# Kernel optimization log

Hardware: AMD Instinct MI355X
Metric: run time of the kernel (lower is better)

Reference implementation:

```python
import jax, jax.numpy as jnp
import numpy as np

# ---- static config (from init_kwargs) ----
B_, L_, DM = 4, 2048, 1024
EXPAND, HEADDIM, DSTATE, DCONV = 2, 64, 64, 7
DIN = EXPAND * DM            # 2048
NH = DIN // HEADDIM          # 32
CONV_DIM = DIN + 2 * DSTATE  # 2176 (x, B, C go through the depthwise conv)
DPROJ = 2 * DIN + 2 * DSTATE + 2 * NH  # 4288 (z, xBC, dt_fwd, dt_bwd)
EPS = 1e-5


def setup_inputs() -> dict:
    key = jax.random.key(0)
    ks = jax.random.split(key, 8)
    s = lambda d: 1.0 / np.sqrt(d)
    # dt_bias = inv_softplus(dt) with dt ~ logUniform(1e-3, 0.1)  (Mamba2/Hydra init)
    dt = jnp.exp(jax.random.uniform(ks[3], (NH,)) * (np.log(0.1) - np.log(0.001)) + np.log(0.001))
    return {
        "x": jax.random.normal(ks[0], (B_, L_, DM), jnp.float32),
        "ln_gamma": jnp.ones((DM,), jnp.float32),
        "ln_beta": jnp.zeros((DM,), jnp.float32),
        "W_in": jax.random.normal(ks[1], (DPROJ, DM), jnp.float32) * s(DM),
        "conv_w": jax.random.normal(ks[2], (CONV_DIM, DCONV), jnp.float32) * s(DCONV),
        "conv_b": jnp.zeros((CONV_DIM,), jnp.float32),
        "dt_bias": jnp.log(jnp.expm1(dt)),
        "A_log": jnp.log(jax.random.uniform(ks[4], (NH,), minval=1.0, maxval=16.0)),
        "fc_D_w": jax.random.normal(ks[5], (NH, DIN), jnp.float32) * s(DIN),
        "D": jnp.ones((NH,), jnp.float32),
        "norm_w": jnp.ones((DIN,), jnp.float32),
        "W_out": jax.random.normal(ks[6], (DM, DIN), jnp.float32) * s(DIN),
    }


def _hydra_layer(x, ln_gamma, ln_beta, W_in, conv_w, conv_b, dt_bias, A_log,
                 fc_D_w, D, norm_w, W_out):
    res = x
    # LayerNorm
    mu = jnp.mean(x, -1, keepdims=True)
    var = jnp.mean((x - mu) ** 2, -1, keepdims=True)
    u = (x - mu) * jax.lax.rsqrt(var + EPS) * ln_gamma + ln_beta

    # input projection -> z (gate), xBC (conv stream), dt (fwd+bwd)
    zxbcdt = jnp.einsum('bld,pd->blp', u, W_in)
    z = zxbcdt[..., :DIN]
    xBC = zxbcdt[..., DIN:DIN + CONV_DIM]
    dt = zxbcdt[..., DIN + CONV_DIM:]               # (B,L,2*NH)

    # depthwise 'same' conv along L + SiLU (bidirectional model -> symmetric pad)
    xBC_c = jax.lax.conv_general_dilated(
        xBC.transpose(0, 2, 1), conv_w[:, None, :], (1,),
        [(DCONV // 2, DCONV // 2)], feature_group_count=CONV_DIM)
    xBC = jax.nn.silu((xBC_c + conv_b[None, :, None]).transpose(0, 2, 1))

    xs = xBC[..., :DIN]                             # (B,L,DIN)
    Bm = xBC[..., DIN:DIN + DSTATE]                 # (B,L,N)
    Cm = xBC[..., DIN + DSTATE:]                    # (B,L,N)

    flip = lambda a: a[:, ::-1]
    # stack forward and (flipped) backward direction along batch
    dt2 = jax.nn.softplus(jnp.concatenate([dt[..., :NH], flip(dt[..., NH:])], 0) + dt_bias)  # (2B,L,NH)
    x2 = jnp.concatenate([xs, flip(xs)], 0).reshape(2 * B_, L_, NH, HEADDIM)
    B2 = jnp.concatenate([Bm, flip(Bm)], 0)
    C2 = jnp.concatenate([Cm, flip(Cm)], 0)

    A = -jnp.exp(A_log)                             # (NH,)
    dA = jnp.exp(dt2 * A)                           # (2B,L,NH)

    # selective SSM recurrence: h_t = dA_t * h_{t-1} + dt_t * x_t B_t^T ; y_t = h_t C_t
    def step(h, inp):
        dA_t, dt_t, B_t, C_t, x_t = inp
        dBx = (dt_t[:, :, None, None] * x_t[..., None]) * B_t[:, None, None, :]
        h = dA_t[:, :, None, None] * h + dBx        # (2B,NH,P,N)
        y = jnp.einsum('bhpn,bn->bhp', h, C_t)
        return h, y

    h0 = jnp.zeros((2 * B_, NH, HEADDIM, DSTATE), x.dtype)
    tr = lambda a: jnp.moveaxis(a, 1, 0)
    _, ys = jax.lax.scan(step, h0, (tr(dA), tr(dt2), tr(B2), tr(C2), tr(x2)))
    y = jnp.moveaxis(ys, 0, 1)                      # (2B,L,NH,P)

    # shift by one: strictly off-diagonal part of the quasiseparable mixing matrix
    y = jnp.concatenate([jnp.zeros_like(y[:, :1]), y[:, :-1]], axis=1)
    y = y[:B_] + flip(y[B_:])                       # (B,L,NH,P)

    # data-dependent diagonal: D(x) = fc_D(x) + D, applied per head
    Ddata = jnp.einsum('bld,hd->blh', xs, fc_D_w) + D
    y = y + xs.reshape(B_, L_, NH, HEADDIM) * Ddata[..., None]
    y = y.reshape(B_, L_, DIN)

    # gated RMSNorm (norm after gate)
    y = y * jax.nn.silu(z)
    y = y * jax.lax.rsqrt(jnp.mean(y * y, -1, keepdims=True) + EPS) * norm_w

    # out proj + residual (dropout is identity in eval)
    return res + jnp.einsum('bli,di->bld', y, W_out)


def reference(x, ln_gamma, ln_beta, W_in, conv_w, conv_b, dt_bias, A_log,
              fc_D_w, D, norm_w, W_out):
    return _hydra_layer(x, ln_gamma, ln_beta, W_in, conv_w, conv_b, dt_bias,
                        A_log, fc_D_w, D, norm_w, W_out)
```

## Files before the change

kernel.cpp:

```cpp
#include <hip/hip_runtime.h>
#include <stdint.h>

#define B_   4
#define L_   2048
#define DM   1024
#define DIN  2048
#define NH   32
#define HD   64
#define DSTATE 64
#define DCONV  7
#define CONV_DIM 2176
#define DPROJ 4288
#define NPAD 4352
#define BL   8192
#define EPS  1e-5f
#define QC   128
#define NCH  16

typedef unsigned short u16;
typedef unsigned int   u32;
typedef __bf16 bf16x8 __attribute__((ext_vector_type(8)));
typedef float  f32x4  __attribute__((ext_vector_type(4)));

__device__ __forceinline__ float b2f(u32 b) { return __uint_as_float(b << 16); }
__device__ __forceinline__ u16 f2b(float f) {
    u32 u = __float_as_uint(f);
    u32 r = (u + 0x7fffu + ((u >> 16) & 1u)) >> 16;
    return (u16)r;
}
__device__ __forceinline__ void unpack8(uint4 v, float* f) {
    f[0] = b2f(v.x & 0xffffu); f[1] = b2f(v.x >> 16);
    f[2] = b2f(v.y & 0xffffu); f[3] = b2f(v.y >> 16);
    f[4] = b2f(v.z & 0xffffu); f[5] = b2f(v.z >> 16);
    f[6] = b2f(v.w & 0xffffu); f[7] = b2f(v.w >> 16);
}
__device__ __forceinline__ uint4 pack8(const float* f) {
    uint4 v;
    v.x = (u32)f2b(f[0]) | ((u32)f2b(f[1]) << 16);
    v.y = (u32)f2b(f[2]) | ((u32)f2b(f[3]) << 16);
    v.z = (u32)f2b(f[4]) | ((u32)f2b(f[5]) << 16);
    v.w = (u32)f2b(f[6]) | ((u32)f2b(f[7]) << 16);
    return v;
}
__device__ __forceinline__ int xts(int p, int s) { return p * 136 + ((p >> 3) << 3) + s; }
__device__ __forceinline__ void gload_lds16(const u16* g, u16* l) {
    __builtin_amdgcn_global_load_lds((const __attribute__((address_space(1))) void*)g,
                                     (__attribute__((address_space(3))) void*)l, 16, 0, 0);
}

__global__ __launch_bounds__(256) void k_cvt_win(const float* __restrict__ W, u16* __restrict__ Wb) {
    int idx = blockIdx.x * 256 + threadIdx.x;
    int n = idx >> 10;
    float v = (n < DPROJ) ? W[(size_t)n * DM + (idx & 1023)] : 0.f;
    Wb[idx] = f2b(v);
}
__global__ __launch_bounds__(256) void k_cvt_wout(const float* __restrict__ W, u16* __restrict__ Wb) {
    int idx = blockIdx.x * 256 + threadIdx.x;
    Wb[idx] = f2b(W[idx]);
}
__global__ __launch_bounds__(256) void k_cvt_fcd(const float* __restrict__ W, u16* __restrict__ Wb) {
    int idx = blockIdx.x * 256 + threadIdx.x;
    Wb[idx] = f2b(W[idx]);
}

__global__ __launch_bounds__(256) void k_ln(const float* __restrict__ x, const float* __restrict__ g,
                                            const float* __restrict__ be, u16* __restrict__ u) {
    int row = blockIdx.x, tid = threadIdx.x;
    const float4* xr = (const float4*)(x + (size_t)row * DM);
    float4 v = xr[tid];
    float s1 = v.x + v.y + v.z + v.w;
    float s2 = v.x * v.x + v.y * v.y + v.z * v.z + v.w * v.w;
    for (int o = 32; o; o >>= 1) { s1 += __shfl_down(s1, o); s2 += __shfl_down(s2, o); }
    __shared__ float ls1[4], ls2[4];
    int w = tid >> 6;
    if ((tid & 63) == 0) { ls1[w] = s1; ls2[w] = s2; }
    __syncthreads();
    float t1 = ls1[0] + ls1[1] + ls1[2] + ls1[3];
    float t2 = ls2[0] + ls2[1] + ls2[2] + ls2[3];
    float mu = t1 * (1.f / DM);
    float var = t2 * (1.f / DM) - mu * mu;
    float rs = rsqrtf(var + EPS);
    float4 gv = ((const float4*)g)[tid];
    float4 bv = ((const float4*)be)[tid];
    float o0 = (v.x - mu) * rs * gv.x + bv.x;
    float o1 = (v.y - mu) * rs * gv.y + bv.y;
    float o2 = (v.z - mu) * rs * gv.z + bv.z;
    float o3 = (v.w - mu) * rs * gv.w + bv.w;
    uint2 p;
    p.x = (u32)f2b(o0) | ((u32)f2b(o1) << 16);
    p.y = (u32)f2b(o2) | ((u32)f2b(o3) << 16);
    ((uint2*)(u + (size_t)row * DM))[tid] = p;
}

__global__ __launch_bounds__(256) void k_gemm_bt(const u16* __restrict__ A, const u16* __restrict__ Bw,
                                                 int M, int N, int K, int out_bf16,
                                                 u16* __restrict__ obf, int ldo,
                                                 float* __restrict__ ofp, const float* __restrict__ res) {
    __shared__ __align__(16) u16 As[128 * 64];
    __shared__ __align__(16) u16 Bs[128 * 64];
    int tid = threadIdx.x;
    int m0 = blockIdx.y * 128, n0 = blockIdx.x * 128;
    int w = tid >> 6, lane = tid & 63;
    int wm = (w >> 1) * 64, wn = (w & 1) * 64;
    int lr = lane & 15, lq = lane >> 4;

    f32x4 acc[4][4];
    #pragma unroll
    for (int i = 0; i < 4; i++)
        #pragma unroll
        for (int j = 0; j < 4; j++) acc[i][j] = (f32x4){0.f, 0.f, 0.f, 0.f};

    for (int kt = 0; kt < K; kt += 64) {
        #pragma unroll
        for (int it = 0; it < 4; it++) {
            int s_idx = it * 256 + tid;
            int row = s_idx >> 3;
            int kcg = (s_idx & 7) ^ (row & 7);
            u16* lbase_a = &As[(it * 256 + w * 64) * 8];
            u16* lbase_b = &Bs[(it * 256 + w * 64) * 8];
            gload_lds16(A + (size_t)(m0 + row) * K + kt + kcg * 8, lbase_a);
            gload_lds16(Bw + (size_t)(n0 + row) * K + kt + kcg * 8, lbase_b);
        }
        __syncthreads();
        #pragma unroll
        for (int kk = 0; kk < 2; kk++) {
            bf16x8 af[4], bfr[4];
            #pragma unroll
            for (int i = 0; i < 4; i++) {
                int row = wm + 16 * i + lr;
                af[i] = *(const bf16x8*)&As[row * 64 + (((kk * 4 + lq)) ^ (row & 7)) * 8];
            }
            #pragma unroll
            for (int j = 0; j < 4; j++) {
                int row = wn + 16 * j + lr;
                bfr[j] = *(const bf16x8*)&Bs[row * 64 + (((kk * 4 + lq)) ^ (row & 7)) * 8];
            }
            #pragma unroll
            for (int i = 0; i < 4; i++)
                #pragma unroll
                for (int j = 0; j < 4; j++)
                    acc[i][j] = __builtin_amdgcn_mfma_f32_16x16x32_bf16(af[i], bfr[j], acc[i][j], 0, 0, 0);
        }
        __syncthreads();
    }
    #pragma unroll
    for (int i = 0; i < 4; i++) {
        #pragma unroll
        for (int j = 0; j < 4; j++) {
            #pragma unroll
            for (int rr = 0; rr < 4; rr++) {
                int m = m0 + wm + 16 * i + lq * 4 + rr;
                int n = n0 + wn + 16 * j + lr;
                float v = acc[i][j][rr];
                if (out_bf16) obf[(size_t)m * ldo + n] = f2b(v);
                else          ofp[(size_t)m * ldo + n] = v + res[(size_t)m * ldo + n];
            }
        }
    }
}

__global__ __launch_bounds__(256) void k_dproj(const u16* __restrict__ xs, const u16* __restrict__ fcb,
                                               const float* __restrict__ Dv, float* __restrict__ Dd) {
    __shared__ __align__(16) u16 As[32 * 72];
    __shared__ __align__(16) u16 Bs[32 * 72];
    int tid = threadIdx.x;
    int m0 = blockIdx.x * 32;
    int w = tid >> 6, lane = tid & 63, lr = lane & 15, lq = lane >> 4;
    int mt = (w & 1) * 16, nt = (w >> 1) * 16;
    int r = tid >> 3, kc = tid & 7;
    f32x4 acc = (f32x4){0.f, 0.f, 0.f, 0.f};
    for (int kt = 0; kt < DIN; kt += 64) {
        *(uint4*)&As[r * 72 + kc * 8] = *(const uint4*)(xs + (size_t)(m0 + r) * DIN + kt + kc * 8);
        *(uint4*)&Bs[r * 72 + kc * 8] = *(const uint4*)(fcb + (size_t)r * DIN + kt + kc * 8);
        __syncthreads();
        #pragma unroll
        for (int ks = 0; ks < 2; ks++) {
            bf16x8 a = *(const bf16x8*)&As[(mt + lr) * 72 + ks * 32 + lq * 8];
            bf16x8 b = *(const bf16x8*)&Bs[(nt + lr) * 72 + ks * 32 + lq * 8];
            acc = __builtin_amdgcn_mfma_f32_16x16x32_bf16(a, b, acc, 0, 0, 0);
        }
        __syncthreads();
    }
    #pragma unroll
    for (int rr = 0; rr < 4; rr++) {
        int m = m0 + mt + lq * 4 + rr;
        int n = nt + lr;
        Dd[(size_t)m * 32 + n] = acc[rr] + Dv[n];
    }
}

__global__ __launch_bounds__(256) void k_conv(const u16* __restrict__ zx, const float* __restrict__ cw,
                                              const float* __restrict__ cb, u16* __restrict__ xs,
                                              u16* __restrict__ BCb) {
    __shared__ u16 sh[262 * 64];
    int c0 = blockIdx.x * 64, t0 = blockIdx.y * 256, b = blockIdx.z;
    int tid = threadIdx.x;
    int c = tid & 63, tg = tid >> 6;
    for (int it = 0; it < 66; it++) {
        int r = it * 4 + tg;
        if (r < 262) {
            int t = t0 + r - 3;
            u16 v = 0;
            if (t >= 0 && t < L_) v = zx[(size_t)(b * L_ + t) * NPAD + DIN + c0 + c];
            sh[r * 64 + c] = v;
        }
    }
    float wgt[7];
    #pragma unroll
    for (int k = 0; k < 7; k++) wgt[k] = cw[(c0 + c) * 7 + k];
    float bias = cb[c0 + c];
    __syncthreads();
    int cg = c0 + c;
    for (int tt = 0; tt < 64; tt++) {
        int tl = tt * 4 + tg;
        float a = bias;
        #pragma unroll
        for (int k = 0; k < 7; k++) a += b2f(sh[(tl + k) * 64 + c]) * wgt[k];
        float v = a / (1.f + __expf(-a));
        size_t row = (size_t)b * L_ + (t0 + tl);
        if (cg < DIN) xs[row * DIN + cg] = f2b(v);
        else          BCb[row * 128 + (cg - DIN)] = f2b(v);
    }
}

__global__ __launch_bounds__(256) void k_chunk(const u16* __restrict__ xs, const u16* __restrict__ BCb,
                                               const u16* __restrict__ zx, const float* __restrict__ dt_bias,
                                               const float* __restrict__ A_log, u16* __restrict__ y0,
                                               u16* __restrict__ y1, float* __restrict__ wout,
                                               float* __restrict__ decay, u16* __restrict__ scb) {
    __shared__ __align__(16) u16 ab[18432];
    __shared__ __align__(16) u16 XT[8768];
    __shared__ __align__(16) u16 BT[8768];
    __shared__ __align__(16) float dts_s[128];
    __shared__ __align__(16) float lda_s[128];
    __shared__ __align__(16) float wend[128];
    __shared__ __align__(16) double cumd[128];

    const int blk = blockIdx.x;
    const int c = blk & 15, dbh = blk >> 4;
    const int h = dbh & 31, b = (dbh >> 5) & 3, dir = dbh >> 7;
    const int tid = threadIdx.x, w = tid >> 6, lane = tid & 63, lr = lane & 15, lq = lane >> 4;
    const int s0 = c * QC;
    u16* yo = dir ? y1 : y0;

    if (tid < 128) {
        int s = s0 + tid;
        int t = dir ? (L_ - 1 - s) : s;
        float draw = b2f(zx[(size_t)(b * L_ + t) * NPAD + (DIN + CONV_DIM) + dir * 32 + h]);
        float xb = draw + dt_bias[h];
        float dt2 = (xb > 20.f) ? xb : log1pf(__expf(xb));
        dts_s[tid] = dt2;
        lda_s[tid] = -__expf(A_log[h]) * dt2;
    }
    {
        int sl0 = tid >> 3, ng = (tid & 7) * 8;
        #pragma unroll
        for (int it = 0; it < 4; it++) {
            int sl = sl0 + it * 32;
            int s = s0 + sl;
            int t = dir ? (L_ - 1 - s) : s;
            size_t row = (size_t)b * L_ + t;
            const u16* bcr = BCb + row * 128;
            uint4 cv = *(const uint4*)(bcr + 64 + ng);
            *(uint4*)&ab[sl * 72 + ng] = cv;
            uint4 pb = *(const uint4*)(bcr + ng);
            *(uint4*)&ab[9216 + sl * 72 + ng] = pb;
            u16 bh[8] = {(u16)(pb.x & 0xffffu), (u16)(pb.x >> 16), (u16)(pb.y & 0xffffu), (u16)(pb.y >> 16),
                         (u16)(pb.z & 0xffffu), (u16)(pb.z >> 16), (u16)(pb.w & 0xffffu), (u16)(pb.w >> 16)};
            #pragma unroll
            for (int i = 0; i < 8; i++) BT[(ng + i) * 136 + ng + sl] = bh[i];
            uint4 xv = *(const uint4*)(xs + row * DIN + h * 64 + ng);
            u16 xh[8] = {(u16)(xv.x & 0xffffu), (u16)(xv.x >> 16), (u16)(xv.y & 0xffffu), (u16)(xv.y >> 16),
                         (u16)(xv.z & 0xffffu), (u16)(xv.z >> 16), (u16)(xv.w & 0xffffu), (u16)(xv.w >> 16)};
            #pragma unroll
            for (int i = 0; i < 8; i++) XT[(ng + i) * 136 + ng + sl] = xh[i];
        }
    }
    __syncthreads();
    if (w == 0) {
        double v0 = (double)lda_s[lane];
        double v1 = (double)lda_s[64 + lane];
        #pragma unroll
        for (int o = 1; o < 64; o <<= 1) {
            double t0 = __shfl_up(v0, o);
            double t1 = __shfl_up(v1, o);
            if (lane >= o) { v0 += t0; v1 += t1; }
        }
        double tot0 = __shfl(v0, 63);
        cumd[lane] = v0;
        cumd[64 + lane] = tot0 + v1;
    }
    bf16x8 af[2][2];
    #pragma unroll
    for (int ti = 0; ti < 2; ti++)
        #pragma unroll
        for (int ks = 0; ks < 2; ks++)
            af[ti][ks] = *(const bf16x8*)&ab[(w * 32 + ti * 16 + lr) * 72 + ks * 32 + lq * 8];
    f32x4 accg[2][8];
    #pragma unroll
    for (int ti = 0; ti < 2; ti++)
        #pragma unroll
        for (int si = 0; si < 8; si++) accg[ti][si] = (f32x4){0.f, 0.f, 0.f, 0.f};
    #pragma unroll
    for (int si = 0; si < 8; si++)
        #pragma unroll
        for (int ks = 0; ks < 2; ks++) {
            bf16x8 bf = *(const bf16x8*)&ab[9216 + (si * 16 + lr) * 72 + ks * 32 + lq * 8];
            accg[0][si] = __builtin_amdgcn_mfma_f32_16x16x32_bf16(af[0][ks], bf, accg[0][si], 0, 0, 0);
            accg[1][si] = __builtin_amdgcn_mfma_f32_16x16x32_bf16(af[1][ks], bf, accg[1][si], 0, 0, 0);
        }
    __syncthreads();
    if (tid < 128) wend[tid] = __expf((float)(cumd[127] - cumd[tid])) * dts_s[tid];
    {
        double cumt_d[8];
        #pragma unroll
        for (int ti = 0; ti < 2; ti++)
            #pragma unroll
            for (int r = 0; r < 4; r++) cumt_d[ti * 4 + r] = cumd[w * 32 + ti * 16 + lq * 4 + r];
        double cums_d[8]; float dts_l[8];
        #pragma unroll
        for (int si = 0; si < 8; si++) { cums_d[si] = cumd[si * 16 + lr]; dts_l[si] = dts_s[si * 16 + lr]; }
        #pragma unroll
        for (int ti = 0; ti < 2; ti++)
            #pragma unroll
            for (int si = 0; si < 8; si++)
                #pragma unroll
                for (int r = 0; r < 4; r++) {
                    int t_l = w * 32 + ti * 16 + lq * 4 + r;
                    int s_l = si * 16 + lr;
                    float v = 0.f;
                    if (s_l <= t_l)
                        v = __expf((float)(cumt_d[ti * 4 + r] - cums_d[si])) * dts_l[si] * accg[ti][si][r];
                    ab[xts(t_l, s_l)] = f2b(v);
                }
    }
    __syncthreads();
    f32x4 acc[2][4];
    #pragma unroll
    for (int ti = 0; ti < 2; ti++)
        #pragma unroll
        for (int pj = 0; pj < 4; pj++) acc[ti][pj] = (f32x4){0.f, 0.f, 0.f, 0.f};
    #pragma unroll
    for (int ks = 0; ks < 4; ks++) {
        bf16x8 a0 = *(const bf16x8*)&ab[xts(w * 32 + lr, ks * 32 + lq * 8)];
        bf16x8 a1 = *(const bf16x8*)&ab[xts(w * 32 + 16 + lr, ks * 32 + lq * 8)];
        #pragma unroll
        for (int pj = 0; pj < 4; pj++) {
            bf16x8 bf = *(const bf16x8*)&XT[xts(pj * 16 + lr, ks * 32 + lq * 8)];
            acc[0][pj] = __builtin_amdgcn_mfma_f32_16x16x32_bf16(a0, bf, acc[0][pj], 0, 0, 0);
            acc[1][pj] = __builtin_amdgcn_mfma_f32_16x16x32_bf16(a1, bf, acc[1][pj], 0, 0, 0);
        }
    }
    __syncthreads();
    #pragma unroll
    for (int ti = 0; ti < 2; ti++)
        #pragma unroll
        for (int pj = 0; pj < 4; pj++)
            #pragma unroll
            for (int r = 0; r < 4; r++) {
                int t_l = w * 32 + ti * 16 + lq * 4 + r;
                ab[t_l * 72 + pj * 16 + lr] = f2b(acc[ti][pj][r]);
            }
    __syncthreads();
    #pragma unroll
    for (int k2 = 0; k2 < 4; k2++) {
        int c2 = k2 * 256 + tid;
        int t_l = c2 >> 3, p0 = (c2 & 7) * 8;
        int s = s0 + t_l;
        int t = dir ? (L_ - 1 - s) : s;
        *(uint4*)(yo + ((size_t)b * L_ + t) * DIN + h * 64 + p0) = *(const uint4*)&ab[t_l * 72 + p0];
    }
    f32x4 accs[4];
    #pragma unroll
    for (int nj = 0; nj < 4; nj++) accs[nj] = (f32x4){0.f, 0.f, 0.f, 0.f};
    #pragma unroll
    for (int ks = 0; ks < 4; ks++) {
        uint4 xv = *(const uint4*)&XT[xts(w * 16 + lr, ks * 32 + lq * 8)];
        float xf[8]; unpack8(xv, xf);
        float4 w0 = *(const float4*)&wend[ks * 32 + lq * 8];
        float4 w1 = *(const float4*)&wend[ks * 32 + lq * 8 + 4];
        float fs[8] = {xf[0]*w0.x, xf[1]*w0.y, xf[2]*w0.z, xf[3]*w0.w,
                       xf[4]*w1.x, xf[5]*w1.y, xf[6]*w1.z, xf[7]*w1.w};
        bf16x8 a = __builtin_bit_cast(bf16x8, pack8(fs));
        #pragma unroll
        for (int nj = 0; nj < 4; nj++) {
            bf16x8 bb = *(const bf16x8*)&BT[xts(nj * 16 + lr, ks * 32 + lq * 8)];
            accs[nj] = __builtin_amdgcn_mfma_f32_16x16x32_bf16(a, bb, accs[nj], 0, 0, 0);
        }
    }
    __syncthreads();
    #pragma unroll
    for (int nj = 0; nj < 4; nj++)
        #pragma unroll
        for (int r = 0; r < 4; r++) {
            int p = w * 16 + lq * 4 + r, n = nj * 16 + lr;
            BT[p * 72 + n] = f2b(accs[nj][r]);
        }
    __syncthreads();
    #pragma unroll
    for (int k2 = 0; k2 < 2; k2++) {
        int c2 = k2 * 256 + tid;
        int p = c2 >> 3, n0 = (c2 & 7) * 8;
        *(uint4*)(scb + (size_t)blk * 4096 + p * 64 + n0) = *(const uint4*)&BT[p * 72 + n0];
    }
    if (tid < 128) wout[dbh * 2048 + s0 + tid] = __expf((float)cumd[tid]);
    if (tid == 0)  decay[blk] = __expf((float)cumd[127]);
}

__global__ __launch_bounds__(256) void k_hscan(const float* __restrict__ decay, u16* __restrict__ scb) {
    int bid = blockIdx.x;
    int dbh = bid >> 2, ps = bid & 3;
    int tid = threadIdx.x;
    u16* base = scb + (size_t)dbh * 16 * 4096 + ps * 1024 + tid * 4;
    float h0 = 0.f, h1 = 0.f, h2 = 0.f, h3 = 0.f;
    for (int c = 0; c < NCH; c++) {
        u16* sg = base + (size_t)c * 4096;
        uint2 q = *(const uint2*)sg;
        float s0 = b2f(q.x & 0xffffu), s1 = b2f(q.x >> 16);
        float s2 = b2f(q.y & 0xffffu), s3 = b2f(q.y >> 16);
        uint2 o;
        o.x = (u32)f2b(h0) | ((u32)f2b(h1) << 16);
        o.y = (u32)f2b(h2) | ((u32)f2b(h3) << 16);
        *(uint2*)sg = o;
        float dk = decay[dbh * 16 + c];
        h0 = dk * h0 + s0; h1 = dk * h1 + s1;
        h2 = dk * h2 + s2; h3 = dk * h3 + s3;
    }
}

__global__ __launch_bounds__(256) void k_inter(const u16* __restrict__ BCb, const float* __restrict__ wout,
                                               const u16* __restrict__ hin, u16* __restrict__ y0,
                                               u16* __restrict__ y1) {
    __shared__ __align__(16) u16 smem[18432];
    u16* Csc = smem;
    u16* hs  = smem + 9216;
    float* fsm = (float*)smem;
    const int blk = blockIdx.x;
    const int c = blk & 15, dbh = blk >> 4;
    const int h = dbh & 31, b = (dbh >> 5) & 3, dir = dbh >> 7;
    const int tid = threadIdx.x, w = tid >> 6, lane = tid & 63, lr = lane & 15, lq = lane >> 4;
    u16* yo = dir ? y1 : y0;

    {
        int g = tid * 16, p = g >> 6, n = g & 63;
        const u16* hg = hin + (size_t)blk * 4096 + g;
        *(uint4*)&hs[p * 72 + n]     = *(const uint4*)hg;
        *(uint4*)&hs[p * 72 + n + 8] = *(const uint4*)(hg + 8);
    }
    const int sl0 = tid >> 3, ng = (tid & 7) * 8;
    #pragma unroll
    for (int it = 0; it < 4; it++) {
        int sl = sl0 + it * 32;
        int s = c * QC + sl;
        int t = dir ? (L_ - 1 - s) : s;
        const u16* bcr = BCb + ((size_t)b * L_ + t) * 128 + 64 + ng;
        float sc = wout[dbh * 2048 + s];
        uint4 cv = *(const uint4*)bcr;
        float cf[8]; unpack8(cv, cf);
        float f[8] = {cf[0]*sc, cf[1]*sc, cf[2]*sc, cf[3]*sc, cf[4]*sc, cf[5]*sc, cf[6]*sc, cf[7]*sc};
        *(uint4*)&Csc[sl * 72 + ng] = pack8(f);
    }
    __syncthreads();
    f32x4 acc[2][4];
    #pragma unroll
    for (int ti = 0; ti < 2; ti++)
        #pragma unroll
        for (int pj = 0; pj < 4; pj++) acc[ti][pj] = (f32x4){0.f, 0.f, 0.f, 0.f};
    #pragma unroll
    for (int ks = 0; ks < 2; ks++) {
        bf16x8 a0 = *(const bf16x8*)&Csc[(w * 32 + lr) * 72 + ks * 32 + lq * 8];
        bf16x8 a1 = *(const bf16x8*)&Csc[(w * 32 + 16 + lr) * 72 + ks * 32 + lq * 8];
        #pragma unroll
        for (int pj = 0; pj < 4; pj++) {
            bf16x8 bb = *(const bf16x8*)&hs[(pj * 16 + lr) * 72 + ks * 32 + lq * 8];
            acc[0][pj] = __builtin_amdgcn_mfma_f32_16x16x32_bf16(a0, bb, acc[0][pj], 0, 0, 0);
            acc[1][pj] = __builtin_amdgcn_mfma_f32_16x16x32_bf16(a1, bb, acc[1][pj], 0, 0, 0);
        }
    }
    __syncthreads();
    #pragma unroll
    for (int ti = 0; ti < 2; ti++)
        #pragma unroll
        for (int pj = 0; pj < 4; pj++)
            #pragma unroll
            for (int r = 0; r < 4; r++) {
                int t_l = w * 32 + ti * 16 + lq * 4 + r;
                fsm[t_l * 68 + pj * 16 + lr] = acc[ti][pj][r];
            }
    __syncthreads();
    #pragma unroll
    for (int k2 = 0; k2 < 4; k2++) {
        int c2 = k2 * 256 + tid;
        int t_l = c2 >> 3, p0 = (c2 & 7) * 8;
        int s = c * QC + t_l;
        int t = dir ? (L_ - 1 - s) : s;
        u16* yp = yo + ((size_t)b * L_ + t) * DIN + h * 64 + p0;
        uint4 ov = *(const uint4*)yp;
        float of[8]; unpack8(ov, of);
        const float4 v0 = *(const float4*)&fsm[t_l * 68 + p0];
        const float4 v1 = *(const float4*)&fsm[t_l * 68 + p0 + 4];
        float nf[8] = {of[0] + v0.x, of[1] + v0.y, of[2] + v0.z, of[3] + v0.w,
                       of[4] + v1.x, of[5] + v1.y, of[6] + v1.z, of[7] + v1.w};
        *(uint4*)yp = pack8(nf);
    }
}

__global__ __launch_bounds__(256) void k_gate(const u16* __restrict__ xs, const u16* __restrict__ zx,
                                              const u16* __restrict__ y0, const u16* __restrict__ y1,
                                              const float* __restrict__ Dd,
                                              const float* __restrict__ nw, u16* __restrict__ yn) {
    int row = blockIdx.x, tid = threadIdx.x;
    int t = row & (L_ - 1);
    __shared__ float red[4];
    size_t base = (size_t)row * DIN;
    uint4 xv = ((const uint4*)(xs + base))[tid];
    uint4 zv = ((const uint4*)(zx + (size_t)row * NPAD))[tid];
    uint4 zero4 = {0u, 0u, 0u, 0u};
    uint4 a0 = (t > 0)      ? ((const uint4*)(y0 + base - DIN))[tid] : zero4;
    uint4 a1 = (t < L_ - 1) ? ((const uint4*)(y1 + base + DIN))[tid] : zero4;
    float sD = Dd[(size_t)row * 32 + (tid >> 3)];
    float xf[8], zf[8], f0[8], f1[8];
    unpack8(xv, xf); unpack8(zv, zf); unpack8(a0, f0); unpack8(a1, f1);
    int d0 = tid * 8;
    float g[8]; float ss = 0.f;
    #pragma unroll
    for (int i = 0; i < 8; i++) {
        float yv = f0[i] + f1[i] + xf[i] * sD;
        float z = zf[i];
        float gg = yv * (z / (1.f + __expf(-z)));
        g[i] = gg; ss += gg * gg;
    }
    for (int o = 32; o; o >>= 1) ss += __shfl_down(ss, o);
    if ((tid & 63) == 0) red[tid >> 6] = ss;
    __syncthreads();
    float tot = red[0] + red[1] + red[2] + red[3];
    float r = rsqrtf(tot * (1.f / DIN) + EPS);
    float o8[8];
    #pragma unroll
    for (int i = 0; i < 8; i++) o8[i] = g[i] * r * nw[d0 + i];
    ((uint4*)(yn + base))[tid] = pack8(o8);
}

#define OFF_U     ((size_t)0)
#define OFF_WIN   ((size_t)16777216)
#define OFF_WOUT  ((size_t)25690112)
#define OFF_ZX    ((size_t)29884416)
#define OFF_XS    ((size_t)101187584)
#define OFF_BC    ((size_t)134742016)
#define OFF_DTA   ((size_t)138936320)
#define OFF_Y0    ((size_t)143130624)
#define OFF_Y1    ((size_t)176685056)
#define OFF_YN    ((size_t)210239488)
#define OFF_WO2   OFF_U
#define OFF_DEC   (OFF_U + 2097152)
#define OFF_FCB   (OFF_U + 2113536)
#define OFF_DD    (OFF_U + 2244608)
#define OFF_SCB   OFF_YN

extern "C" void kernel_launch(void* const* d_in, const int* in_sizes, int n_in,
                              void* d_out, int out_size, void* d_ws, size_t ws_size,
                              hipStream_t stream) {
    const float* x       = (const float*)d_in[0];
    const float* ln_g    = (const float*)d_in[1];
    const float* ln_b    = (const float*)d_in[2];
    const float* W_in    = (const float*)d_in[3];
    const float* conv_w  = (const float*)d_in[4];
    const float* conv_b  = (const float*)d_in[5];
    const float* dt_bias = (const float*)d_in[6];
    const float* A_log   = (const float*)d_in[7];
    const float* fc_D_w  = (const float*)d_in[8];
    const float* Dv      = (const float*)d_in[9];
    const float* norm_w  = (const float*)d_in[10];
    const float* W_out   = (const float*)d_in[11];

    char* ws = (char*)d_ws;
    u16*   u_bf  = (u16*)(ws + OFF_U);
    u16*   winb  = (u16*)(ws + OFF_WIN);
    u16*   woutb = (u16*)(ws + OFF_WOUT);
    u16*   zx    = (u16*)(ws + OFF_ZX);
    u16*   xs    = (u16*)(ws + OFF_XS);
    u16*   BCb   = (u16*)(ws + OFF_BC);
    u16*   y0b   = (u16*)(ws + OFF_Y0);
    u16*   y1b   = (u16*)(ws + OFF_Y1);
    u16*   ynb   = (u16*)(ws + OFF_YN);
    float* wo2   = (float*)(ws + OFF_WO2);
    float* dec   = (float*)(ws + OFF_DEC);
    u16*   fcb   = (u16*)(ws + OFF_FCB);
    float* Dd    = (float*)(ws + OFF_DD);
    u16*   scb   = (u16*)(ws + OFF_SCB);

    k_cvt_win <<<(NPAD * DM) / 256, 256, 0, stream>>>(W_in, winb);
    k_cvt_wout<<<(DM * DIN) / 256, 256, 0, stream>>>(W_out, woutb);
    k_ln      <<<BL, 256, 0, stream>>>(x, ln_g, ln_b, u_bf);
    k_gemm_bt <<<dim3(NPAD / 128, BL / 128), 256, 0, stream>>>(u_bf, winb, BL, NPAD, DM, 1, zx, NPAD, nullptr, nullptr);
    k_cvt_fcd <<<(NH * DIN) / 256, 256, 0, stream>>>(fc_D_w, fcb);
    k_conv    <<<dim3(CONV_DIM / 64, L_ / 256, B_), 256, 0, stream>>>(zx, conv_w, conv_b, xs, BCb);
    k_dproj   <<<BL / 32, 256, 0, stream>>>(xs, fcb, Dv, Dd);
    k_chunk   <<<4096, 256, 0, stream>>>(xs, BCb, zx, dt_bias, A_log, y0b, y1b, wo2, dec, scb);
    k_hscan   <<<1024, 256, 0, stream>>>(dec, scb);
    k_inter   <<<4096, 256, 0, stream>>>(BCb, wo2, scb, y0b, y1b);
    k_gate    <<<BL, 256, 0, stream>>>(xs, zx, y0b, y1b, Dd, norm_w, ynb);
    k_gemm_bt <<<dim3(DM / 128, BL / 128), 256, 0, stream>>>(ynb, woutb, BL, DM, DIN, 0, nullptr, DM, (float*)d_out, x);
}
```

Baseline: 520.6 us.

## Vectorize weight conversions, split-K dproj with atomics, merge chunk epilogue syncs

The weight-conversion kernels now handle four floats per thread with float4 loads and packed bf16 stores, which cuts the grid size and per-element overhead. The D projection is split along K into 8 slices across a second grid dimension. Each slice accumulates into Dd with atomicAdd, and a new init kernel pre-fills Dd with the D bias. This raises the block count for a small kernel (256 blocks), in exchange for atomic traffic and one extra launch. The chunk kernel's y and state epilogues now share one LDS round-trip, which drops two barriers.

Result: no change. 519.3 us (-0.2%).

```diff
diff --git a/kernel.cpp b/kernel.cpp
--- a/kernel.cpp
+++ b/kernel.cpp
@@ -49,18 +49,32 @@
 }
 
 __global__ __launch_bounds__(256) void k_cvt_win(const float* __restrict__ W, u16* __restrict__ Wb) {
-    int idx = blockIdx.x * 256 + threadIdx.x;
-    int n = idx >> 10;
-    float v = (n < DPROJ) ? W[(size_t)n * DM + (idx & 1023)] : 0.f;
-    Wb[idx] = f2b(v);
+    int idx4 = (blockIdx.x * 256 + threadIdx.x) * 4;
+    int n = idx4 >> 10;
+    int col = idx4 & 1023;
+    uint2 p = {0u, 0u};
+    if (n < DPROJ) {
+        float4 v = *(const float4*)(W + (size_t)n * DM + col);
+        p.x = (u32)f2b(v.x) | ((u32)f2b(v.y) << 16);
+        p.y = (u32)f2b(v.z) | ((u32)f2b(v.w) << 16);
+    }
+    *(uint2*)(Wb + idx4) = p;
 }
 __global__ __launch_bounds__(256) void k_cvt_wout(const float* __restrict__ W, u16* __restrict__ Wb) {
-    int idx = blockIdx.x * 256 + threadIdx.x;
-    Wb[idx] = f2b(W[idx]);
+    int idx4 = (blockIdx.x * 256 + threadIdx.x) * 4;
+    float4 v = *(const float4*)(W + idx4);
+    uint2 p;
+    p.x = (u32)f2b(v.x) | ((u32)f2b(v.y) << 16);
+    p.y = (u32)f2b(v.z) | ((u32)f2b(v.w) << 16);
+    *(uint2*)(Wb + idx4) = p;
 }
 __global__ __launch_bounds__(256) void k_cvt_fcd(const float* __restrict__ W, u16* __restrict__ Wb) {
-    int idx = blockIdx.x * 256 + threadIdx.x;
-    Wb[idx] = f2b(W[idx]);
+    int idx4 = (blockIdx.x * 256 + threadIdx.x) * 4;
+    float4 v = *(const float4*)(W + idx4);
+    uint2 p;
+    p.x = (u32)f2b(v.x) | ((u32)f2b(v.y) << 16);
+    p.y = (u32)f2b(v.z) | ((u32)f2b(v.w) << 16);
+    *(uint2*)(Wb + idx4) = p;
 }
 
 __global__ __launch_bounds__(256) void k_ln(const float* __restrict__ x, const float* __restrict__ g,
@@ -159,17 +173,23 @@
     }
 }
 
+__global__ __launch_bounds__(256) void k_dzero(const float* __restrict__ Dv, float* __restrict__ Dd) {
+    int idx = blockIdx.x * 256 + threadIdx.x;
+    Dd[idx] = Dv[idx & 31];
+}
+
 __global__ __launch_bounds__(256) void k_dproj(const u16* __restrict__ xs, const u16* __restrict__ fcb,
-                                               const float* __restrict__ Dv, float* __restrict__ Dd) {
+                                               float* __restrict__ Dd) {
     __shared__ __align__(16) u16 As[32 * 72];
     __shared__ __align__(16) u16 Bs[32 * 72];
     int tid = threadIdx.x;
     int m0 = blockIdx.x * 32;
+    int k0 = blockIdx.y * 256;
     int w = tid >> 6, lane = tid & 63, lr = lane & 15, lq = lane >> 4;
     int mt = (w & 1) * 16, nt = (w >> 1) * 16;
     int r = tid >> 3, kc = tid & 7;
     f32x4 acc = (f32x4){0.f, 0.f, 0.f, 0.f};
-    for (int kt = 0; kt < DIN; kt += 64) {
+    for (int kt = k0; kt < k0 + 256; kt += 64) {
         *(uint4*)&As[r * 72 + kc * 8] = *(const uint4*)(xs + (size_t)(m0 + r) * DIN + kt + kc * 8);
         *(uint4*)&Bs[r * 72 + kc * 8] = *(const uint4*)(fcb + (size_t)r * DIN + kt + kc * 8);
         __syncthreads();
@@ -185,7 +205,7 @@
     for (int rr = 0; rr < 4; rr++) {
         int m = m0 + mt + lq * 4 + rr;
         int n = nt + lr;
-        Dd[(size_t)m * 32 + n] = acc[rr] + Dv[n];
+        atomicAdd(&Dd[(size_t)m * 32 + n], acc[rr]);
     }
 }
 
@@ -351,25 +371,6 @@
             acc[1][pj] = __builtin_amdgcn_mfma_f32_16x16x32_bf16(a1, bf, acc[1][pj], 0, 0, 0);
         }
     }
-    __syncthreads();
-    #pragma unroll
-    for (int ti = 0; ti < 2; ti++)
-        #pragma unroll
-        for (int pj = 0; pj < 4; pj++)
-            #pragma unroll
-            for (int r = 0; r < 4; r++) {
-                int t_l = w * 32 + ti * 16 + lq * 4 + r;
-                ab[t_l * 72 + pj * 16 + lr] = f2b(acc[ti][pj][r]);
-            }
-    __syncthreads();
-    #pragma unroll
-    for (int k2 = 0; k2 < 4; k2++) {
-        int c2 = k2 * 256 + tid;
-        int t_l = c2 >> 3, p0 = (c2 & 7) * 8;
-        int s = s0 + t_l;
-        int t = dir ? (L_ - 1 - s) : s;
-        *(uint4*)(yo + ((size_t)b * L_ + t) * DIN + h * 64 + p0) = *(const uint4*)&ab[t_l * 72 + p0];
-    }
     f32x4 accs[4];
     #pragma unroll
     for (int nj = 0; nj < 4; nj++) accs[nj] = (f32x4){0.f, 0.f, 0.f, 0.f};
@@ -390,6 +391,15 @@
     }
     __syncthreads();
     #pragma unroll
+    for (int ti = 0; ti < 2; ti++)
+        #pragma unroll
+        for (int pj = 0; pj < 4; pj++)
+            #pragma unroll
+            for (int r = 0; r < 4; r++) {
+                int t_l = w * 32 + ti * 16 + lq * 4 + r;
+                ab[t_l * 72 + pj * 16 + lr] = f2b(acc[ti][pj][r]);
+            }
+    #pragma unroll
     for (int nj = 0; nj < 4; nj++)
         #pragma unroll
         for (int r = 0; r < 4; r++) {
@@ -397,6 +407,14 @@
             BT[p * 72 + n] = f2b(accs[nj][r]);
         }
     __syncthreads();
+    #pragma unroll
+    for (int k2 = 0; k2 < 4; k2++) {
+        int c2 = k2 * 256 + tid;
+        int t_l = c2 >> 3, p0 = (c2 & 7) * 8;
+        int s = s0 + t_l;
+        int t = dir ? (L_ - 1 - s) : s;
+        *(uint4*)(yo + ((size_t)b * L_ + t) * DIN + h * 64 + p0) = *(const uint4*)&ab[t_l * 72 + p0];
+    }
     #pragma unroll
     for (int k2 = 0; k2 < 2; k2++) {
         int c2 = k2 * 256 + tid;
@@ -589,13 +607,14 @@
     float* Dd    = (float*)(ws + OFF_DD);
     u16*   scb   = (u16*)(ws + OFF_SCB);
 
-    k_cvt_win <<<(NPAD * DM) / 256, 256, 0, stream>>>(W_in, winb);
-    k_cvt_wout<<<(DM * DIN) / 256, 256, 0, stream>>>(W_out, woutb);
+    k_cvt_win <<<(NPAD * DM) / 1024, 256, 0, stream>>>(W_in, winb);
+    k_cvt_wout<<<(DM * DIN) / 1024, 256, 0, stream>>>(W_out, woutb);
     k_ln      <<<BL, 256, 0, stream>>>(x, ln_g, ln_b, u_bf);
     k_gemm_bt <<<dim3(NPAD / 128, BL / 128), 256, 0, stream>>>(u_bf, winb, BL, NPAD, DM, 1, zx, NPAD, nullptr, nullptr);
-    k_cvt_fcd <<<(NH * DIN) / 256, 256, 0, stream>>>(fc_D_w, fcb);
+    k_cvt_fcd <<<(NH * DIN) / 1024, 256, 0, stream>>>(fc_D_w, fcb);
+    k_dzero   <<<(BL * 32) / 256, 256, 0, stream>>>(Dv, Dd);
     k_conv    <<<dim3(CONV_DIM / 64, L_ / 256, B_), 256, 0, stream>>>(zx, conv_w, conv_b, xs, BCb);
-    k_dproj   <<<BL / 32, 256, 0, stream>>>(xs, fcb, Dv, Dd);
+    k_dproj   <<<dim3(BL / 32, 8), 256, 0, stream>>>(xs, fcb, Dd);
     k_chunk   <<<4096, 256, 0, stream>>>(xs, BCb, zx, dt_bias, A_log, y0b, y1b, wo2, dec, scb);
     k_hscan   <<<1024, 256, 0, stream>>>(dec, scb);
     k_inter   <<<4096, 256, 0, stream>>>(BCb, wo2, scb, y0b, y1b);
```
